# Performance work log

Hardware: AMD Instinct MI355X
Metric: run time of the kernel (lower is better)

## Reference

```python
import jax, jax.numpy as jnp
import numpy as np

QN, QP = -8, 7  # signed 4-bit


def round_pass(x):
    # straight-through round (forward: round-half-even like torch.round)
    return x + jax.lax.stop_gradient(jnp.round(x) - x)


def setup_inputs() -> dict:
    key = jax.random.key(0)
    ks = jax.random.split(key, 9)
    B, S, D, H = 16, 1024, 768, 3072
    def unif(k, shape):
        return jax.random.uniform(k, shape, jnp.float32, 0.02, 0.1)
    return {
        "x0": jax.random.normal(ks[0], (B, S, D), jnp.float32),
        "w1": jax.random.normal(ks[1], (H, D), jnp.float32) * 0.02,
        "b1": jax.random.normal(ks[2], (H,), jnp.float32) * 0.02,
        "alpha_w1": unif(ks[3], (H,)),
        "alpha_a1": unif(ks[4], (D,)),
        "w2": jax.random.normal(ks[5], (D, H), jnp.float32) * 0.02,
        "b2": jax.random.normal(ks[6], (D,), jnp.float32) * 0.02,
        "alpha_w2": unif(ks[7], (D,)),
        "alpha_a2": unif(ks[8], (H,)),
    }


def _quant_act(x, alpha_a):
    # ActQ_v2: per-tensor (mean of kernel-wise alpha), signed int4
    a = alpha_a.mean()
    return round_pass(jnp.clip(x / a, QN, QP))


def _quant_w(w, alpha_w):
    # LinearQ_v2: per-output-channel alpha, shape [out, in]
    return round_pass(jnp.clip(w / alpha_w[:, None], QN, QP))


def reference(x0, w1, b1, alpha_w1, alpha_a1, w2, b2, alpha_w2, alpha_a2):
    # fc1: int4 act quant, int4 weight quant, integer matmul, dequant scale + bias
    xq = _quant_act(x0, alpha_a1)                       # [B,S,D] integer-valued
    wq1 = _quant_w(w1, alpha_w1)                        # [H,D] integer-valued
    x1 = jnp.einsum('bsd,hd->bsh', xq, wq1)             # int matmul (float carrier)
    x1 = x1 * alpha_w1 * alpha_a1.mean() + b1           # per-channel dequant + bias
    x1 = jax.nn.gelu(x1, approximate=False)             # nn.GELU (exact erf)
    x1 = jnp.clip(x1, -10.0, 10.0)
    # dropout p=0.0 -> identity
    # fc2
    hq = _quant_act(x1, alpha_a2)                       # [B,S,H]
    wq2 = _quant_w(w2, alpha_w2)                        # [D,H]
    x2 = jnp.einsum('bsh,dh->bsd', hq, wq2)
    x2 = x2 * alpha_w2 * alpha_a2.mean() + b2
    return x2
```

## Files before the change

kernel.cpp:

```cpp
#include <hip/hip_runtime.h>
#include <hip/hip_bf16.h>
#include <math.h>


typedef __attribute__((ext_vector_type(4))) int i32x4;

__device__ __forceinline__ void gload_lds16(const void* g, void* l) {
  __builtin_amdgcn_global_load_lds(
      (const __attribute__((address_space(1))) void*)g,
      (__attribute__((address_space(3))) void*)l, 16, 0, 0);
}

__device__ __forceinline__ int q4_i8(float x, float a) {
  float t = x / a;
  t = fminf(fmaxf(t, -8.0f), 7.0f);
  t = rintf(t);
  return (int)t;
}

__global__ void means_k(const float* __restrict__ v1, int n1,
                        const float* __restrict__ v2, int n2,
                        float* __restrict__ out) {
  const float* src = blockIdx.x ? v2 : v1;
  const int n = blockIdx.x ? n2 : n1;
  __shared__ double red[256];
  double s = 0.0;
  for (int i = threadIdx.x; i < n; i += 256) s += (double)src[i];
  red[threadIdx.x] = s;
  __syncthreads();
  for (int st = 128; st > 0; st >>= 1) {
    if (threadIdx.x < st) red[threadIdx.x] += red[threadIdx.x + st];
    __syncthreads();
  }
  if (threadIdx.x == 0) {
    float m = (float)(red[0] / (double)n);
    out[blockIdx.x] = m;
    if (blockIdx.x == 1) {
      out[2] = 1.0f / m;
      out[3] = 0.5f * (1.0f / m);
    }
  }
}

__global__ void quant_x_k(const float* __restrict__ x,
                          unsigned* __restrict__ xq,
                          const float* __restrict__ means, int n4) {
  int i = blockIdx.x * blockDim.x + threadIdx.x;
  if (i >= n4) return;
  const float a = means[0];
  float4 v = ((const float4*)x)[i];
  unsigned u = (q4_i8(v.x, a) & 0xFF) | ((q4_i8(v.y, a) & 0xFF) << 8) |
               ((q4_i8(v.z, a) & 0xFF) << 16) | ((q4_i8(v.w, a) & 0xFF) << 24);
  xq[i] = u;
}

__global__ void quant_w_k(const float* __restrict__ w,
                          const float* __restrict__ alpha,
                          unsigned* __restrict__ wq, int C, int n4) {
  int i = blockIdx.x * blockDim.x + threadIdx.x;
  if (i >= n4) return;
  int row = (i * 4) / C;
  const float a = alpha[row];
  float4 v = ((const float4*)w)[i];
  unsigned u = (q4_i8(v.x, a) & 0xFF) | ((q4_i8(v.y, a) & 0xFF) << 8) |
               ((q4_i8(v.z, a) & 0xFF) << 16) | ((q4_i8(v.w, a) & 0xFF) << 24);
  wq[i] = u;
}

__global__ __launch_bounds__(512, 8) void gemm1_k(
    const signed char* __restrict__ A, const signed char* __restrict__ B,
    const float* __restrict__ alphaw, const float* __restrict__ bias,
    const float* __restrict__ means, signed char* __restrict__ out_b, int N,
    int K) {
  __shared__ __align__(16) signed char sA[128 * 128];
  __shared__ __align__(16) signed char sB[128 * 128];
  const int tid = threadIdx.x;
  const int w = tid >> 6;
  const int l = tid & 63;
  const int wm = w >> 1, wn = w & 1;
  const long bm0 = (long)blockIdx.y * 128;
  const long bn0 = (long)blockIdx.x * 128;

  i32x4 acc[2][4] = {};

  const int srow = l >> 3;
  const int scol = ((l & 7) * 16) ^ (srow << 4);
  const int rsw = (l & 7) << 4;

  const signed char* gA = A + (bm0 + w * 16 + srow) * (long)K + scol;
  const signed char* gB = B + (bn0 + w * 16 + srow) * (long)K + scol;

  for (int kt = 0; kt < K; kt += 128) {
    __syncthreads();
#pragma unroll
    for (int i = 0; i < 2; ++i) {
      gload_lds16(gA + (long)i * 8 * K + kt, &sA[(w * 2 + i) * 1024]);
      gload_lds16(gB + (long)i * 8 * K + kt, &sB[(w * 2 + i) * 1024]);
    }
    __syncthreads();
#pragma unroll
    for (int kk = 0; kk < 2; ++kk) {
      const int kc = (kk * 64 + (l >> 4) * 16) ^ rsw;
      i32x4 af[2], bg[4];
#pragma unroll
      for (int m = 0; m < 2; ++m)
        af[m] = *(const i32x4*)&sA[(wm * 32 + m * 16 + (l & 15)) * 128 + kc];
#pragma unroll
      for (int n = 0; n < 4; ++n)
        bg[n] = *(const i32x4*)&sB[(wn * 64 + n * 16 + (l & 15)) * 128 + kc];
#pragma unroll
      for (int m = 0; m < 2; ++m)
#pragma unroll
        for (int n = 0; n < 4; ++n)
          acc[m][n] = __builtin_amdgcn_mfma_i32_16x16x64_i8(af[m], bg[n],
                                                            acc[m][n], 0, 0, 0);
    }
  }

  const float a1 = means[0];
  const float half_inv_a2 = means[3];

  float awa1[4], bsc[4];
  const int cc0 = (int)bn0 + wn * 64 + (l & 15);
#pragma unroll
  for (int n = 0; n < 4; ++n) {
    awa1[n] = alphaw[cc0 + n * 16] * a1;
    bsc[n] = bias[cc0 + n * 16];
  }

  const int r0 = (int)bm0 + wm * 32 + (l >> 4) * 4;

#pragma unroll
  for (int m = 0; m < 2; ++m) {
#pragma unroll
    for (int rg = 0; rg < 4; ++rg) {
      const int r = r0 + m * 16 + rg;
      signed char* prow = out_b + (size_t)r * N + cc0;
#pragma unroll
      for (int n = 0; n < 4; ++n) {
        const float f = (float)acc[m][n][rg];
        const float t = fmaf(f, awa1[n], bsc[n]);
        const float x = t * 0.70710678118654752f;
        const float az = fabsf(x);
        const float rr = __builtin_amdgcn_rcpf(fmaf(0.3275911f, az, 1.0f));
        float p = fmaf(rr, 1.061405429f, -1.453152027f);
        p = fmaf(rr, p, 1.421413741f);
        p = fmaf(rr, p, -0.284496736f);
        p = fmaf(rr, p, 0.254829592f);
        p = p * rr;
        const float e = __expf(-az * az);
        float er = fmaf(-p, e, 1.0f);
        er = copysignf(er, x);
        float qv = t * (1.0f + er) * half_inv_a2;
        qv = fminf(fmaxf(qv, -8.0f), 7.0f);
        qv = rintf(qv);
        prow[n * 16] = (signed char)(int)qv;
      }
    }
  }
}

__global__ __launch_bounds__(512, 6) void gemm2_k(
    const signed char* __restrict__ A, const signed char* __restrict__ B,
    const float* __restrict__ alphaw, const float* __restrict__ bias,
    const float* __restrict__ means, float* __restrict__ out_f, int N, int K) {
  __shared__ __align__(16) signed char sA[128 * 128];
  __shared__ __align__(16) signed char sB[128 * 128];
  const int tid = threadIdx.x;
  const int w = tid >> 6;
  const int l = tid & 63;
  const int wm = w >> 1, wn = w & 1;
  const long bm0 = (long)blockIdx.y * 128;
  const long bn0 = (long)blockIdx.x * 128;

  i32x4 acc[2][4] = {};

  const int srow = l >> 3;
  const int scol = ((l & 7) * 16) ^ (srow << 4);
  const int rsw = (l & 7) << 4;

  const signed char* gA = A + (bm0 + w * 16 + srow) * (long)K + scol;
  const signed char* gB = B + (bn0 + w * 16 + srow) * (long)K + scol;

  for (int kt = 0; kt < K; kt += 128) {
    __syncthreads();
#pragma unroll
    for (int i = 0; i < 2; ++i) {
      gload_lds16(gA + (long)i * 8 * K + kt, &sA[(w * 2 + i) * 1024]);
      gload_lds16(gB + (long)i * 8 * K + kt, &sB[(w * 2 + i) * 1024]);
    }
    __syncthreads();
#pragma unroll
    for (int kk = 0; kk < 2; ++kk) {
      const int kc = (kk * 64 + (l >> 4) * 16) ^ rsw;
      i32x4 af[2], bg[4];
#pragma unroll
      for (int m = 0; m < 2; ++m)
        af[m] = *(const i32x4*)&sA[(wm * 32 + m * 16 + (l & 15)) * 128 + kc];
#pragma unroll
      for (int n = 0; n < 4; ++n)
        bg[n] = *(const i32x4*)&sB[(wn * 64 + n * 16 + (l & 15)) * 128 + kc];
#pragma unroll
      for (int m = 0; m < 2; ++m)
#pragma unroll
        for (int n = 0; n < 4; ++n)
          acc[m][n] = __builtin_amdgcn_mfma_i32_16x16x64_i8(af[m], bg[n],
                                                            acc[m][n], 0, 0, 0);
    }
  }

  const float a2 = means[1];

  float awc[4], bsc[4];
  const int cc0 = (int)bn0 + wn * 64 + (l & 15);
#pragma unroll
  for (int n = 0; n < 4; ++n) {
    awc[n] = alphaw[cc0 + n * 16];
    bsc[n] = bias[cc0 + n * 16];
  }

  const int r0 = (int)bm0 + wm * 32 + (l >> 4) * 4;

#pragma unroll
  for (int m = 0; m < 2; ++m) {
#pragma unroll
    for (int rg = 0; rg < 4; ++rg) {
      const int r = r0 + m * 16 + rg;
      float* prow = out_f + (size_t)r * N + cc0;
#pragma unroll
      for (int n = 0; n < 4; ++n) {
        const float f = (float)acc[m][n][rg];
        float t = __fmul_rn(f, awc[n]);
        t = __fmul_rn(t, a2);
        t = __fadd_rn(t, bsc[n]);
        prow[n * 16] = t;
      }
    }
  }
}

extern "C" void kernel_launch(void* const* d_in, const int* in_sizes, int n_in,
                              void* d_out, int out_size, void* d_ws,
                              size_t ws_size, hipStream_t stream) {
  const float* x0 = (const float*)d_in[0];
  const float* w1 = (const float*)d_in[1];
  const float* b1 = (const float*)d_in[2];
  const float* aw1 = (const float*)d_in[3];
  const float* aa1 = (const float*)d_in[4];
  const float* w2 = (const float*)d_in[5];
  const float* b2 = (const float*)d_in[6];
  const float* aw2 = (const float*)d_in[7];
  const float* aa2 = (const float*)d_in[8];

  char* ws = (char*)d_ws;
  float* means = (float*)ws;
  signed char* xq = (signed char*)(ws + 256);
  signed char* wq1 = (signed char*)(ws + 12583168);
  signed char* wq2 = (signed char*)(ws + 14942464);
  signed char* hq = (signed char*)(ws + 17301760);

  means_k<<<2, 256, 0, stream>>>(aa1, 768, aa2, 3072, means);
  quant_x_k<<<12288, 256, 0, stream>>>(x0, (unsigned*)xq, means, 3145728);
  quant_w_k<<<2304, 256, 0, stream>>>(w1, aw1, (unsigned*)wq1, 768, 589824);
  quant_w_k<<<2304, 256, 0, stream>>>(w2, aw2, (unsigned*)wq2, 3072, 589824);
  dim3 g1(24, 128);
  gemm1_k<<<g1, 512, 0, stream>>>(xq, wq1, aw1, b1, means, hq, 3072, 768);
  dim3 g2(6, 128);
  gemm2_k<<<g2, 512, 0, stream>>>(hq, wq2, aw2, b2, means, (float*)d_out, 768,
                                  3072);
}
```

Measured before the change: 144.1 us.

## Double-buffer LDS tiles in gemm1 with compile-time K and tighter GELU epilogue

```diff
diff --git a/kernel.cpp b/kernel.cpp
--- a/kernel.cpp
+++ b/kernel.cpp
@@ -67,13 +67,16 @@
   wq[i] = u;
 }
 
-__global__ __launch_bounds__(512, 8) void gemm1_k(
+template <int NT>
+__global__ __launch_bounds__(512, 4) void gemm1_k(
     const signed char* __restrict__ A, const signed char* __restrict__ B,
     const float* __restrict__ alphaw, const float* __restrict__ bias,
-    const float* __restrict__ means, signed char* __restrict__ out_b, int N,
-    int K) {
-  __shared__ __align__(16) signed char sA[128 * 128];
-  __shared__ __align__(16) signed char sB[128 * 128];
+    const float* __restrict__ means, signed char* __restrict__ out_b, int N) {
+  constexpr int K = NT * 128;
+  __shared__ __align__(16) signed char sA0[128 * 128];
+  __shared__ __align__(16) signed char sB0[128 * 128];
+  __shared__ __align__(16) signed char sA1[128 * 128];
+  __shared__ __align__(16) signed char sB1[128 * 128];
   const int tid = threadIdx.x;
   const int w = tid >> 6;
   const int l = tid & 63;
@@ -90,24 +93,24 @@
   const signed char* gA = A + (bm0 + w * 16 + srow) * (long)K + scol;
   const signed char* gB = B + (bn0 + w * 16 + srow) * (long)K + scol;
 
-  for (int kt = 0; kt < K; kt += 128) {
-    __syncthreads();
+  auto STAGE = [&](signed char* dA, signed char* dB, int kt) {
 #pragma unroll
     for (int i = 0; i < 2; ++i) {
-      gload_lds16(gA + (long)i * 8 * K + kt, &sA[(w * 2 + i) * 1024]);
-      gload_lds16(gB + (long)i * 8 * K + kt, &sB[(w * 2 + i) * 1024]);
-    }
-    __syncthreads();
+      gload_lds16(gA + (long)i * 8 * K + kt, dA + (w * 2 + i) * 1024);
+      gload_lds16(gB + (long)i * 8 * K + kt, dB + (w * 2 + i) * 1024);
+    }
+  };
+  auto COMPUTE = [&](const signed char* pA, const signed char* pB) {
 #pragma unroll
     for (int kk = 0; kk < 2; ++kk) {
       const int kc = (kk * 64 + (l >> 4) * 16) ^ rsw;
       i32x4 af[2], bg[4];
 #pragma unroll
       for (int m = 0; m < 2; ++m)
-        af[m] = *(const i32x4*)&sA[(wm * 32 + m * 16 + (l & 15)) * 128 + kc];
+        af[m] = *(const i32x4*)&pA[(wm * 32 + m * 16 + (l & 15)) * 128 + kc];
 #pragma unroll
       for (int n = 0; n < 4; ++n)
-        bg[n] = *(const i32x4*)&sB[(wn * 64 + n * 16 + (l & 15)) * 128 + kc];
+        bg[n] = *(const i32x4*)&pB[(wn * 64 + n * 16 + (l & 15)) * 128 + kc];
 #pragma unroll
       for (int m = 0; m < 2; ++m)
 #pragma unroll
@@ -115,6 +118,25 @@
           acc[m][n] = __builtin_amdgcn_mfma_i32_16x16x64_i8(af[m], bg[n],
                                                             acc[m][n], 0, 0, 0);
     }
+  };
+
+  STAGE(sA0, sB0, 0);
+#pragma unroll
+  for (int T = 0; T < NT; T += 2) {
+    STAGE(sA1, sB1, (T + 1) * 128);
+    asm volatile("s_waitcnt vmcnt(4)" ::: "memory");
+    __builtin_amdgcn_s_barrier();
+    COMPUTE(sA0, sB0);
+    __builtin_amdgcn_s_barrier();
+    if (T + 2 < NT) {
+      STAGE(sA0, sB0, (T + 2) * 128);
+      asm volatile("s_waitcnt vmcnt(4)" ::: "memory");
+    } else {
+      asm volatile("s_waitcnt vmcnt(0)" ::: "memory");
+    }
+    __builtin_amdgcn_s_barrier();
+    COMPUTE(sA1, sB1);
+    __builtin_amdgcn_s_barrier();
   }
 
   const float a1 = means[0];
@@ -141,18 +163,19 @@
         const float f = (float)acc[m][n][rg];
         const float t = fmaf(f, awa1[n], bsc[n]);
         const float x = t * 0.70710678118654752f;
-        const float az = fabsf(x);
-        const float rr = __builtin_amdgcn_rcpf(fmaf(0.3275911f, az, 1.0f));
+        const float den = fmaf(0.3275911f, fabsf(x), 1.0f);
+        const float rr = __builtin_amdgcn_rcpf(den);
         float p = fmaf(rr, 1.061405429f, -1.453152027f);
         p = fmaf(rr, p, 1.421413741f);
         p = fmaf(rr, p, -0.284496736f);
         p = fmaf(rr, p, 0.254829592f);
-        p = p * rr;
-        const float e = __expf(-az * az);
-        float er = fmaf(-p, e, 1.0f);
+        const float q = p * rr;
+        const float e = __expf(-(x * x));
+        float er = fmaf(-q, e, 1.0f);
         er = copysignf(er, x);
-        float qv = t * (1.0f + er) * half_inv_a2;
-        qv = fminf(fmaxf(qv, -8.0f), 7.0f);
+        const float g2 = fmaf(er, t, t);
+        float qv = g2 * half_inv_a2;
+        qv = __builtin_amdgcn_fmed3f(qv, -8.0f, 7.0f);
         qv = rintf(qv);
         prow[n * 16] = (signed char)(int)qv;
       }
@@ -264,7 +287,7 @@
   quant_w_k<<<2304, 256, 0, stream>>>(w1, aw1, (unsigned*)wq1, 768, 589824);
   quant_w_k<<<2304, 256, 0, stream>>>(w2, aw2, (unsigned*)wq2, 3072, 589824);
   dim3 g1(24, 128);
-  gemm1_k<<<g1, 512, 0, stream>>>(xq, wq1, aw1, b1, means, hq, 3072, 768);
+  gemm1_k<6><<<g1, 512, 0, stream>>>(xq, wq1, aw1, b1, means, hq, 3072);
   dim3 g2(6, 128);
   gemm2_k<<<g2, 512, 0, stream>>>(hq, wq2, aw2, b2, means, (float*)d_out, 768,
                                   3072);
```

Result: faster. 141.1 us (-2.1%).
